# Optimization experiments

Hardware: AMD Instinct MI355X
Metric: run time of the kernel (lower is better)

Reference implementation:

```python
import jax, jax.numpy as jnp
import numpy as np

# spk_param = (thr, temp, damp); dt, tau from module config
THR, TEMP, DAMP = 0.4, 0.1, 0.9
DT, TAU = 0.1, 1.0


@jax.custom_vjp
def spike(v, u):
    # Stochastic Bernoulli spike: sigmoid(temp*v) > uniform noise
    return (jax.nn.sigmoid(TEMP * v) > u).astype(v.dtype)

def _spike_fwd(v, u):
    return spike(v, u), v

def _spike_bwd(v, g):
    # Faithful to the torch Spike.backward: returns the pseudo-derivative
    # damp*clamp(1-|v|,0) directly (the original ignores grad_output).
    return (DAMP * jnp.maximum(1.0 - jnp.abs(v), 0.0), jnp.zeros_like(v))

spike.defvjp(_spike_fwd, _spike_bwd)


def setup_inputs() -> dict:
    key = jax.random.key(0)
    k1, k2, k3, k4, k5 = jax.random.split(key, 5)
    B_, T, IN, N, OUT = 128, 512, 128, 512, 128
    inputs = jax.random.normal(k1, (B_, T, IN), dtype=jnp.float32)
    rand_u = jax.random.uniform(k2, (B_, T, N), dtype=jnp.float32)
    init_std = 1.0
    J = jax.random.normal(k3, (N, N), dtype=jnp.float32) * (init_std / np.sqrt(N))
    Bw = jax.random.normal(k4, (N, IN), dtype=jnp.float32)  # input projection (non-trainable in torch)
    W = jax.random.normal(k5, (OUT, N), dtype=jnp.float32) * (1.0 / np.sqrt(N))
    return {"inputs": inputs, "rand_u": rand_u, "J": J, "Bw": Bw, "W": W}


def reference(inputs, rand_u, J, Bw, W):
    B_, T, _ = inputs.shape
    N = J.shape[0]
    alpha = DT / TAU
    decay = 1.0 - alpha

    def step(carry, xs):
        v, z = carry
        x_t, u_t = xs  # [B, IN], [B, N]
        v_new = decay * v + alpha * z
        lamb = jnp.tanh(v_new) @ J.T + x_t @ Bw.T  # [B, N]
        z_new = spike((lamb - THR) / THR, u_t)
        out = lamb @ W.T  # [B, OUT]
        return (v_new, z_new), (v_new, z_new, out)

    v0 = jnp.zeros((B_, N), dtype=inputs.dtype)
    z0 = jnp.zeros((B_, N), dtype=inputs.dtype)
    xs = (jnp.swapaxes(inputs, 0, 1), jnp.swapaxes(rand_u, 0, 1))  # time-major
    _, (vs, zs, outs) = jax.lax.scan(step, (v0, z0), xs)

    vt = jnp.concatenate([v0[:, None, :], jnp.swapaxes(vs, 0, 1)], axis=1)  # [B, T+1, N]
    zt = jnp.concatenate([z0[:, None, :], jnp.swapaxes(zs, 0, 1)], axis=1)  # [B, T+1, N]
    output_seq = jnp.swapaxes(outs, 0, 1)  # [B, T, OUT]
    return vt, zt, output_seq
```

## Files before the change

kernel.cpp:

```cpp
#include <hip/hip_runtime.h>


typedef __attribute__((ext_vector_type(8))) short short8x;
typedef __attribute__((ext_vector_type(4))) float f32x4;

#define OFF_JQK  (0u)
#define OFF_BWH  (262144u)
#define OFF_BWL  (393216u)
#define OFF_G    (524288u)
#define OFF_M    (786432u)
#define OFF_GPK  (851968u)
#define OFF_MPK  (983040u)

#define SC_J 640.0f
#define SC_S 166.0f

__device__ __forceinline__ unsigned short f2bf(float f) {
  union { float f; unsigned u; } a; a.f = f;
  unsigned r = a.u + 0x7FFFu + ((a.u >> 16) & 1u);
  return (unsigned short)(r >> 16);
}
__device__ __forceinline__ float bf2f(unsigned short h) {
  union { unsigned u; float f; } a; a.u = ((unsigned)h) << 16;
  return a.f;
}
__device__ __forceinline__ float thr_of(float u) {
  return __builtin_fmaf(4.0f, __logf(u / (1.0f - u)), 0.4f);
}
__device__ __forceinline__ float fast_tanh_pos(float x) {
  const float e2 = __expf(x + x);
  return 1.0f - 2.0f / (e2 + 1.0f);
}
__device__ __forceinline__ int sdot4(unsigned a, unsigned b, int acc) {
#if __has_builtin(__builtin_amdgcn_sdot4)
  return __builtin_amdgcn_sdot4((int)a, (int)b, acc, false);
#else
  int r;
  asm("v_dot4_i32_i8 %0, %1, %2, %3" : "=v"(r) : "v"(a), "v"(b), "v"(acc));
  return r;
#endif
}
template <int CTRL>
__device__ __forceinline__ int dpp_add(int x) {
  return x + __builtin_amdgcn_update_dpp(0, x, CTRL, 0xF, 0xF, true);
}
__device__ __forceinline__ int dpp_reduce8(int x) {
  return dpp_add<0x141>(dpp_add<0x4E>(dpp_add<0xB1>(x)));
}

__launch_bounds__(512)
__global__ void jwm_kernel(const float* __restrict__ J, const float* __restrict__ Bw,
                           const float* __restrict__ W, unsigned char* __restrict__ ws) {
  __shared__ float wrow[512];
  const int o = blockIdx.x;
  const int tid = threadIdx.x;
  wrow[tid] = W[(size_t)o * 512 + tid];
  __syncthreads();
  const int k = tid, i = tid & 127;
  float g = 0.0f, m = 0.0f;
  for (int n = 0; n < 512; ++n) {
    const float wv = wrow[n];
    g = __builtin_fmaf(wv, J[(size_t)n * 512 + k], g);
    m = __builtin_fmaf(wv, Bw[(size_t)n * 128 + i], m);
  }
  ((float*)(ws + OFF_G))[(size_t)o * 512 + k] = g;
  if (tid < 128) ((float*)(ws + OFF_M))[(size_t)o * 128 + i] = m;
}

__global__ void pack_kernel(const float* __restrict__ J, const float* __restrict__ Bw,
                            unsigned char* __restrict__ ws) {
  const int id = blockIdx.x * 256 + threadIdx.x;
  if (id < 16384) {
    const int f = id;
    const int l = f & 63, j = (f >> 6) & 3, i = (f >> 8) & 7, w = f >> 11;
    const int kap = l & 7;
    const int n = w * 64 + (l >> 3) * 8 + i;
    const int k0 = 64 * kap + 16 * j;
    unsigned dw[4];
#pragma unroll
    for (int d = 0; d < 4; ++d) {
      unsigned x = 0;
#pragma unroll
      for (int p = 0; p < 4; ++p) {
        const float jv = J[(size_t)n * 512 + k0 + 4 * d + p];
        int q = __float2int_rn(jv * SC_J);
        q = q > 127 ? 127 : (q < -127 ? -127 : q);
        x |= ((unsigned)(q & 255)) << (8 * p);
      }
      dw[d] = x;
    }
    uint4 out; out.x = dw[0]; out.y = dw[1]; out.z = dw[2]; out.w = dw[3];
    ((uint4*)(ws + OFF_JQK))[f] = out;
  } else if (id < 24576) {
    const int idx = id - 16384;
    const int n = idx & 511, kg = idx >> 9, k0 = kg * 8;
    unsigned short* bwh = (unsigned short*)(ws + OFF_BWH);
    unsigned short* bwl = (unsigned short*)(ws + OFF_BWL);
    for (int e = 0; e < 8; ++e) {
      const float x = Bw[(size_t)n * 128 + k0 + e];
      const unsigned short h = f2bf(x);
      bwh[(size_t)idx * 8 + e] = h;
      bwl[(size_t)idx * 8 + e] = f2bf(x - bf2f(h));
    }
  } else if (id < 32768) {
    const int idx = id - 24576;
    const int o = idx & 127, kg = idx >> 7, k0 = kg * 8;
    const float* G = (const float*)(ws + OFF_G);
    unsigned short* gpk = (unsigned short*)(ws + OFF_GPK);
    for (int e = 0; e < 8; ++e) gpk[(size_t)idx * 8 + e] = f2bf(G[(size_t)o * 512 + k0 + e]);
  } else {
    const int idx = id - 32768;
    const int o = idx & 127, kg = idx >> 7, k0 = kg * 8;
    const float* M = (const float*)(ws + OFF_M);
    unsigned short* mpk = (unsigned short*)(ws + OFF_MPK);
    for (int e = 0; e < 8; ++e) mpk[(size_t)idx * 8 + e] = f2bf(M[(size_t)o * 128 + k0 + e]);
  }
}

__launch_bounds__(256)
__global__ void xpd_kernel(const float* __restrict__ X, const float* __restrict__ U,
                           const unsigned char* __restrict__ ws, float* __restrict__ Dbuf) {
  __shared__ short Ah[64 * 136];
  __shared__ short Al[64 * 136];
  const unsigned short* bwh = (const unsigned short*)(ws + OFF_BWH);
  const unsigned short* bwl = (const unsigned short*)(ws + OFF_BWL);
  const int m0 = blockIdx.x * 64;
  const int n0 = blockIdx.y * 64;
  const int tid = threadIdx.x;
  for (int i = tid; i < 64 * 32; i += 256) {
    const int r = i >> 5, kq = i & 31;
    const float4 x4 = *(const float4*)(X + (size_t)(m0 + r) * 128 + kq * 4);
    short4 h4, l4; unsigned short h;
    h = f2bf(x4.x); h4.x = (short)h; l4.x = (short)f2bf(x4.x - bf2f(h));
    h = f2bf(x4.y); h4.y = (short)h; l4.y = (short)f2bf(x4.y - bf2f(h));
    h = f2bf(x4.z); h4.z = (short)h; l4.z = (short)f2bf(x4.z - bf2f(h));
    h = f2bf(x4.w); h4.w = (short)h; l4.w = (short)f2bf(x4.w - bf2f(h));
    *(short4*)(&Ah[r * 136 + kq * 4]) = h4;
    *(short4*)(&Al[r * 136 + kq * 4]) = l4;
  }
  __syncthreads();
  const int w = tid >> 6, l = tid & 63, lhi = l >> 4, llo = l & 15;
  const int rowA = 16 * w + llo;
  f32x4 a0 = {0,0,0,0}, a1 = {0,0,0,0}, a2 = {0,0,0,0}, a3 = {0,0,0,0};
#pragma unroll
  for (int kt = 0; kt < 4; ++kt) {
    const short8x ah = *(const short8x*)(&Ah[rowA * 136 + kt * 32 + lhi * 8]);
    const short8x al = *(const short8x*)(&Al[rowA * 136 + kt * 32 + lhi * 8]);
#define XT(TI, ACC) { \
    const size_t bi = ((size_t)((kt * 4 + lhi) * 512 + n0 + TI * 16 + llo)) * 8; \
    const short8x bh = *(const short8x*)(bwh + bi); \
    const short8x bl = *(const short8x*)(bwl + bi); \
    ACC = __builtin_amdgcn_mfma_f32_16x16x32_bf16(ah, bh, ACC, 0, 0, 0); \
    ACC = __builtin_amdgcn_mfma_f32_16x16x32_bf16(al, bh, ACC, 0, 0, 0); \
    ACC = __builtin_amdgcn_mfma_f32_16x16x32_bf16(ah, bl, ACC, 0, 0, 0); }
    XT(0, a0) XT(1, a1) XT(2, a2) XT(3, a3)
#undef XT
  }
  const int n = n0 + llo;
#pragma unroll
  for (int r = 0; r < 4; ++r) {
    const int bt = m0 + 16 * w + lhi * 4 + r;
    const int bb = bt >> 9, tt = bt & 511;
    const float* urow = U + (size_t)bt * 512;
    float* drow = Dbuf + ((size_t)bb * 513 + tt + 1) * 512;
    drow[n]      = thr_of(urow[n])      - a0[r];
    drow[n + 16] = thr_of(urow[n + 16]) - a1[r];
    drow[n + 32] = thr_of(urow[n + 32]) - a2[r];
    drow[n + 48] = thr_of(urow[n + 48]) - a3[r];
  }
}

__launch_bounds__(512, 1)
__global__ void fused_kernel(const float* __restrict__ X, unsigned char* __restrict__ ws,
                             float* __restrict__ vt, float* __restrict__ zt,
                             float* __restrict__ op) {
  __shared__ __align__(16) unsigned char s_sm[2][640];
  __shared__ unsigned short sl[64 * 520];
  __shared__ unsigned short xl[64 * 136];
  const int b = blockIdx.x;
  const int tid = threadIdx.x;
  const int w = tid >> 6, l = tid & 63;
  const int kap = l & 7, kap80 = kap * 80;
  const int lhi = l >> 4, llo = l & 15;

  uint4 jr[8][4];
#pragma unroll
  for (int i = 0; i < 8; ++i)
#pragma unroll
    for (int j = 0; j < 4; ++j) {
      const unsigned char* p = ws + OFF_JQK +
          (size_t)(((w * 8 + i) * 4 + j) * 64 + l) * 16;
      asm volatile("global_load_dwordx4 %0, %1, off" : "=v"(jr[i][j]) : "v"(p));
    }
  asm volatile("s_waitcnt vmcnt(0)" ::: "memory");

  const unsigned short* gpk = (const unsigned short*)(ws + OFF_GPK);
  const unsigned short* mpk = (const unsigned short*)(ws + OFF_MPK);
  const float SC = 1.0f / (SC_J * SC_S);

  vt[((size_t)b * 513) * 512 + tid] = 0.0f;
  zt[((size_t)b * 513) * 512 + tid] = 0.0f;

  const float* Dp = vt + ((size_t)b * 513 + 1) * 512 + tid;
  float* vtw = vt + ((size_t)b * 513 + 1) * 512 + tid;
  float* ztw = zt + ((size_t)b * 513 + 1) * 512 + tid;

  float dc[8], dnx[8];
#pragma unroll
  for (int i = 0; i < 8; ++i) dc[i] = Dp[(size_t)i * 512];

  unsigned zprev = 0u;
  float v0 = 0.0f, v1 = 0.1f;
  float sf0 = fast_tanh_pos(v0), sf1 = fast_tanh_pos(v1);
  unsigned q0 = (unsigned)__float2int_rn(sf0 * SC_S);
  unsigned q1 = (unsigned)__float2int_rn(sf1 * SC_S);

  for (int C = 0; C < 8; ++C) {
#pragma unroll 1
    for (int c = 0; c < 8; ++c) {
      const int t0 = C * 64 + c * 8;
#pragma unroll
      for (int i = 0; i < 8; ++i) dnx[i] = Dp[(size_t)(t0 + 8 + i) * 512];
#pragma unroll
      for (int i = 0; i < 8; ++i) {
        const int t = t0 + i;
        const int tl = t & 63;
        const unsigned q = zprev ? q1 : q0;
        const float v = zprev ? v1 : v0;
        const float sf = zprev ? sf1 : sf0;
        s_sm[t & 1][w * 80 + l] = (unsigned char)q;
        sl[tl * 520 + tid] = f2bf(sf);
        asm volatile("s_waitcnt lgkmcnt(0)\n\ts_barrier" ::: "memory");
        v0 = 0.9f * v; v1 = v0 + 0.1f;
        sf0 = fast_tanh_pos(v0); sf1 = fast_tanh_pos(v1);
        q0 = (unsigned)__float2int_rn(sf0 * SC_S);
        q1 = (unsigned)__float2int_rn(sf1 * SC_S);
        const unsigned char* sb = &s_sm[t & 1][0];
        const uint4 s0 = *(const uint4*)(sb + kap80);
        const uint4 s1 = *(const uint4*)(sb + kap80 + 16);
        const uint4 s2 = *(const uint4*)(sb + kap80 + 32);
        const uint4 s3 = *(const uint4*)(sb + kap80 + 48);
        int a0 = 0, a1 = 0, a2 = 0, a3 = 0, a4 = 0, a5 = 0, a6 = 0, a7 = 0;
#define DOT(AI, I) \
        AI = sdot4(jr[I][0].x, s0.x, AI); AI = sdot4(jr[I][0].y, s0.y, AI); \
        AI = sdot4(jr[I][0].z, s0.z, AI); AI = sdot4(jr[I][0].w, s0.w, AI); \
        AI = sdot4(jr[I][1].x, s1.x, AI); AI = sdot4(jr[I][1].y, s1.y, AI); \
        AI = sdot4(jr[I][1].z, s1.z, AI); AI = sdot4(jr[I][1].w, s1.w, AI); \
        AI = sdot4(jr[I][2].x, s2.x, AI); AI = sdot4(jr[I][2].y, s2.y, AI); \
        AI = sdot4(jr[I][2].z, s2.z, AI); AI = sdot4(jr[I][2].w, s2.w, AI); \
        AI = sdot4(jr[I][3].x, s3.x, AI); AI = sdot4(jr[I][3].y, s3.y, AI); \
        AI = sdot4(jr[I][3].z, s3.z, AI); AI = sdot4(jr[I][3].w, s3.w, AI);
        DOT(a0, 0) DOT(a1, 1) DOT(a2, 2) DOT(a3, 3)
        DOT(a4, 4) DOT(a5, 5) DOT(a6, 6) DOT(a7, 7)
#undef DOT
        a0 = dpp_reduce8(a0); a1 = dpp_reduce8(a1);
        a2 = dpp_reduce8(a2); a3 = dpp_reduce8(a3);
        a4 = dpp_reduce8(a4); a5 = dpp_reduce8(a5);
        a6 = dpp_reduce8(a6); a7 = dpp_reduce8(a7);
        const int q01 = (l & 1) ? a1 : a0;
        const int q23 = (l & 1) ? a3 : a2;
        const int q45 = (l & 1) ? a5 : a4;
        const int q67 = (l & 1) ? a7 : a6;
        const int r0 = (l & 2) ? q23 : q01;
        const int r1 = (l & 2) ? q67 : q45;
        const int accv = (l & 4) ? r1 : r0;
        const float lam = (float)accv * SC;
        const unsigned z = (lam > dc[i]) ? 1u : 0u;
        unsigned zzero;
        asm("v_and_b32 %0, 0, %1" : "=v"(zzero) : "v"(z));
        vtw[(size_t)t * 512 + zzero] = v;
        ztw[(size_t)t * 512] = z ? 1.0f : 0.0f;
        zprev = z;
      }
#pragma unroll
      for (int i = 0; i < 8; ++i) dc[i] = dnx[i];
    }
    float4 xr[4];
#pragma unroll
    for (int i = 0; i < 4; ++i) {
      const int idx = i * 512 + tid;
      const int r = idx >> 5, c4 = (idx & 31) * 4;
      xr[i] = *(const float4*)(X + ((size_t)b * 512 + C * 64 + r) * 128 + c4);
    }
#pragma unroll
    for (int i = 0; i < 4; ++i) {
      const int idx = i * 512 + tid;
      const int r = idx >> 5, c4 = (idx & 31) * 4;
      short4 h4;
      h4.x = (short)f2bf(xr[i].x); h4.y = (short)f2bf(xr[i].y);
      h4.z = (short)f2bf(xr[i].z); h4.w = (short)f2bf(xr[i].w);
      *(short4*)(xl + r * 136 + c4) = h4;
    }
    __syncthreads();
    const int m = w >> 1, oh = (w & 1) * 4;
    f32x4 a0 = {0,0,0,0}, a1 = {0,0,0,0}, a2 = {0,0,0,0}, a3 = {0,0,0,0};
#pragma unroll
    for (int kt = 0; kt < 16; ++kt) {
      const short8x A = *(const short8x*)(sl + (m * 16 + llo) * 520 + kt * 32 + lhi * 8);
#define GT(TI, ACC) { \
      const short8x B = *(const short8x*)(gpk + ((size_t)((kt * 4 + lhi) * 128 + (oh + TI) * 16 + llo)) * 8); \
      ACC = __builtin_amdgcn_mfma_f32_16x16x32_bf16(A, B, ACC, 0, 0, 0); }
      GT(0, a0) GT(1, a1) GT(2, a2) GT(3, a3)
#undef GT
    }
#pragma unroll
    for (int kt = 0; kt < 4; ++kt) {
      const short8x A = *(const short8x*)(xl + (m * 16 + llo) * 136 + kt * 32 + lhi * 8);
#define MT(TI, ACC) { \
      const short8x B = *(const short8x*)(mpk + ((size_t)((kt * 4 + lhi) * 128 + (oh + TI) * 16 + llo)) * 8); \
      ACC = __builtin_amdgcn_mfma_f32_16x16x32_bf16(A, B, ACC, 0, 0, 0); }
      MT(0, a0) MT(1, a1) MT(2, a2) MT(3, a3)
#undef MT
    }
    float* obase = op + ((size_t)b * 512 + C * 64 + m * 16 + lhi * 4) * 128 + llo;
#pragma unroll
    for (int r = 0; r < 4; ++r) {
      float* orow = obase + (size_t)r * 128;
      orow[(oh + 0) * 16] = a0[r];
      orow[(oh + 1) * 16] = a1[r];
      orow[(oh + 2) * 16] = a2[r];
      orow[(oh + 3) * 16] = a3[r];
    }
    __syncthreads();
  }
}

extern "C" void kernel_launch(void* const* d_in, const int* in_sizes, int n_in,
                              void* d_out, int out_size, void* d_ws, size_t ws_size,
                              hipStream_t stream) {
  const float* X  = (const float*)d_in[0];
  const float* U  = (const float*)d_in[1];
  const float* J  = (const float*)d_in[2];
  const float* Bw = (const float*)d_in[3];
  const float* W  = (const float*)d_in[4];
  float* vt = (float*)d_out;
  float* zt = vt + (size_t)128 * 513 * 512;
  float* op = vt + (size_t)2 * 128 * 513 * 512;
  unsigned char* ws = (unsigned char*)d_ws;

  jwm_kernel<<<128, 512, 0, stream>>>(J, Bw, W, ws);
  pack_kernel<<<136, 256, 0, stream>>>(J, Bw, ws);
  xpd_kernel<<<dim3(1024, 8), 256, 0, stream>>>(X, U, ws, vt);
  fused_kernel<<<128, 512, 0, stream>>>(X, ws, vt, zt, op);
}
```

Before: 803.2 us.

## Split output projection out of recurrence into a separate parallel MFMA kernel

```diff
diff --git a/kernel.cpp b/kernel.cpp
--- a/kernel.cpp
+++ b/kernel.cpp
@@ -171,17 +171,14 @@
 }
 
 __launch_bounds__(512, 1)
-__global__ void fused_kernel(const float* __restrict__ X, unsigned char* __restrict__ ws,
-                             float* __restrict__ vt, float* __restrict__ zt,
-                             float* __restrict__ op) {
+__global__ void recur_kernel(const unsigned char* __restrict__ ws,
+                             const float* __restrict__ Dv,
+                             float* __restrict__ vtw, float* __restrict__ ztw) {
   __shared__ __align__(16) unsigned char s_sm[2][640];
-  __shared__ unsigned short sl[64 * 520];
-  __shared__ unsigned short xl[64 * 136];
   const int b = blockIdx.x;
   const int tid = threadIdx.x;
   const int w = tid >> 6, l = tid & 63;
   const int kap = l & 7, kap80 = kap * 80;
-  const int lhi = l >> 4, llo = l & 15;
 
   uint4 jr[8][4];
 #pragma unroll
@@ -194,134 +191,142 @@
     }
   asm volatile("s_waitcnt vmcnt(0)" ::: "memory");
 
+  const float SC = 1.0f / (SC_J * SC_S);
+  vtw[((size_t)b * 513) * 512 + tid] = 0.0f;
+  ztw[((size_t)b * 513) * 512 + tid] = 0.0f;
+
+  const float* Dp = Dv + ((size_t)b * 513 + 1) * 512 + tid;
+  float* vbase = vtw + ((size_t)b * 513 + 1) * 512 + tid;
+  float* zbase = ztw + ((size_t)b * 513 + 1) * 512 + tid;
+
+  float dc[8], dnx[8];
+#pragma unroll
+  for (int i = 0; i < 8; ++i) dc[i] = Dp[(size_t)i * 512];
+
+  unsigned zprev = 0u;
+  float v0 = 0.0f, v1 = 0.1f;
+  unsigned q0 = (unsigned)__float2int_rn(fast_tanh_pos(v0) * SC_S);
+  unsigned q1 = (unsigned)__float2int_rn(fast_tanh_pos(v1) * SC_S);
+
+  for (int c = 0; c < 64; ++c) {
+    const int t0 = c * 8;
+#pragma unroll
+    for (int i = 0; i < 8; ++i) dnx[i] = Dp[(size_t)(t0 + 8 + i) * 512];
+    float v_arr[8];
+    unsigned zbits = 0u;
+#pragma unroll
+    for (int i = 0; i < 8; ++i) {
+      const int t = t0 + i;
+      const unsigned q = zprev ? q1 : q0;
+      const float v = zprev ? v1 : v0;
+      v_arr[i] = v;
+      s_sm[t & 1][w * 80 + l] = (unsigned char)q;
+      asm volatile("s_waitcnt lgkmcnt(0)\n\ts_barrier" ::: "memory");
+      v0 = 0.9f * v; v1 = v0 + 0.1f;
+      q0 = (unsigned)__float2int_rn(fast_tanh_pos(v0) * SC_S);
+      q1 = (unsigned)__float2int_rn(fast_tanh_pos(v1) * SC_S);
+      const unsigned char* sb = &s_sm[t & 1][0];
+      const uint4 s0 = *(const uint4*)(sb + kap80);
+      const uint4 s1 = *(const uint4*)(sb + kap80 + 16);
+      const uint4 s2 = *(const uint4*)(sb + kap80 + 32);
+      const uint4 s3 = *(const uint4*)(sb + kap80 + 48);
+      int a0 = 0, a1 = 0, a2 = 0, a3 = 0, a4 = 0, a5 = 0, a6 = 0, a7 = 0;
+#define DOT(AI, I) \
+      AI = sdot4(jr[I][0].x, s0.x, AI); AI = sdot4(jr[I][0].y, s0.y, AI); \
+      AI = sdot4(jr[I][0].z, s0.z, AI); AI = sdot4(jr[I][0].w, s0.w, AI); \
+      AI = sdot4(jr[I][1].x, s1.x, AI); AI = sdot4(jr[I][1].y, s1.y, AI); \
+      AI = sdot4(jr[I][1].z, s1.z, AI); AI = sdot4(jr[I][1].w, s1.w, AI); \
+      AI = sdot4(jr[I][2].x, s2.x, AI); AI = sdot4(jr[I][2].y, s2.y, AI); \
+      AI = sdot4(jr[I][2].z, s2.z, AI); AI = sdot4(jr[I][2].w, s2.w, AI); \
+      AI = sdot4(jr[I][3].x, s3.x, AI); AI = sdot4(jr[I][3].y, s3.y, AI); \
+      AI = sdot4(jr[I][3].z, s3.z, AI); AI = sdot4(jr[I][3].w, s3.w, AI);
+      DOT(a0, 0) DOT(a1, 1) DOT(a2, 2) DOT(a3, 3)
+      DOT(a4, 4) DOT(a5, 5) DOT(a6, 6) DOT(a7, 7)
+#undef DOT
+      a0 = dpp_reduce8(a0); a1 = dpp_reduce8(a1);
+      a2 = dpp_reduce8(a2); a3 = dpp_reduce8(a3);
+      a4 = dpp_reduce8(a4); a5 = dpp_reduce8(a5);
+      a6 = dpp_reduce8(a6); a7 = dpp_reduce8(a7);
+      const int q01 = (l & 1) ? a1 : a0;
+      const int q23 = (l & 1) ? a3 : a2;
+      const int q45 = (l & 1) ? a5 : a4;
+      const int q67 = (l & 1) ? a7 : a6;
+      const int r0 = (l & 2) ? q23 : q01;
+      const int r1 = (l & 2) ? q67 : q45;
+      const int accv = (l & 4) ? r1 : r0;
+      const float lam = (float)accv * SC;
+      const unsigned z = (lam > dc[i]) ? 1u : 0u;
+      zbits |= z << i;
+      zprev = z;
+    }
+    unsigned zzero;
+    asm("v_and_b32 %0, 0, %1" : "=v"(zzero) : "v"(zprev));
+    float* vst = vbase + (size_t)t0 * 512 + zzero;
+    float* zst = zbase + (size_t)t0 * 512;
+#pragma unroll
+    for (int i = 0; i < 8; ++i) {
+      vst[(size_t)i * 512] = v_arr[i];
+      zst[(size_t)i * 512] = ((zbits >> i) & 1u) ? 1.0f : 0.0f;
+    }
+#pragma unroll
+    for (int i = 0; i < 8; ++i) dc[i] = dnx[i];
+  }
+}
+
+__launch_bounds__(512)
+__global__ void outk_kernel(const float* __restrict__ X, const float* __restrict__ vt,
+                            const unsigned char* __restrict__ ws,
+                            float* __restrict__ op) {
+  __shared__ unsigned short sl[64 * 520];
+  __shared__ unsigned short xl[64 * 136];
+  const int m0 = blockIdx.x * 64;
+  const int tid = threadIdx.x;
+  const int w = tid >> 6, l = tid & 63, lhi = l >> 4, llo = l & 15;
   const unsigned short* gpk = (const unsigned short*)(ws + OFF_GPK);
   const unsigned short* mpk = (const unsigned short*)(ws + OFF_MPK);
-  const float SC = 1.0f / (SC_J * SC_S);
-
-  vt[((size_t)b * 513) * 512 + tid] = 0.0f;
-  zt[((size_t)b * 513) * 512 + tid] = 0.0f;
-
-  const float* Dp = vt + ((size_t)b * 513 + 1) * 512 + tid;
-  float* vtw = vt + ((size_t)b * 513 + 1) * 512 + tid;
-  float* ztw = zt + ((size_t)b * 513 + 1) * 512 + tid;
-
-  float dc[8], dnx[8];
-#pragma unroll
-  for (int i = 0; i < 8; ++i) dc[i] = Dp[(size_t)i * 512];
-
-  unsigned zprev = 0u;
-  float v0 = 0.0f, v1 = 0.1f;
-  float sf0 = fast_tanh_pos(v0), sf1 = fast_tanh_pos(v1);
-  unsigned q0 = (unsigned)__float2int_rn(sf0 * SC_S);
-  unsigned q1 = (unsigned)__float2int_rn(sf1 * SC_S);
-
-  for (int C = 0; C < 8; ++C) {
-#pragma unroll 1
-    for (int c = 0; c < 8; ++c) {
-      const int t0 = C * 64 + c * 8;
-#pragma unroll
-      for (int i = 0; i < 8; ++i) dnx[i] = Dp[(size_t)(t0 + 8 + i) * 512];
-#pragma unroll
-      for (int i = 0; i < 8; ++i) {
-        const int t = t0 + i;
-        const int tl = t & 63;
-        const unsigned q = zprev ? q1 : q0;
-        const float v = zprev ? v1 : v0;
-        const float sf = zprev ? sf1 : sf0;
-        s_sm[t & 1][w * 80 + l] = (unsigned char)q;
-        sl[tl * 520 + tid] = f2bf(sf);
-        asm volatile("s_waitcnt lgkmcnt(0)\n\ts_barrier" ::: "memory");
-        v0 = 0.9f * v; v1 = v0 + 0.1f;
-        sf0 = fast_tanh_pos(v0); sf1 = fast_tanh_pos(v1);
-        q0 = (unsigned)__float2int_rn(sf0 * SC_S);
-        q1 = (unsigned)__float2int_rn(sf1 * SC_S);
-        const unsigned char* sb = &s_sm[t & 1][0];
-        const uint4 s0 = *(const uint4*)(sb + kap80);
-        const uint4 s1 = *(const uint4*)(sb + kap80 + 16);
-        const uint4 s2 = *(const uint4*)(sb + kap80 + 32);
-        const uint4 s3 = *(const uint4*)(sb + kap80 + 48);
-        int a0 = 0, a1 = 0, a2 = 0, a3 = 0, a4 = 0, a5 = 0, a6 = 0, a7 = 0;
-#define DOT(AI, I) \
-        AI = sdot4(jr[I][0].x, s0.x, AI); AI = sdot4(jr[I][0].y, s0.y, AI); \
-        AI = sdot4(jr[I][0].z, s0.z, AI); AI = sdot4(jr[I][0].w, s0.w, AI); \
-        AI = sdot4(jr[I][1].x, s1.x, AI); AI = sdot4(jr[I][1].y, s1.y, AI); \
-        AI = sdot4(jr[I][1].z, s1.z, AI); AI = sdot4(jr[I][1].w, s1.w, AI); \
-        AI = sdot4(jr[I][2].x, s2.x, AI); AI = sdot4(jr[I][2].y, s2.y, AI); \
-        AI = sdot4(jr[I][2].z, s2.z, AI); AI = sdot4(jr[I][2].w, s2.w, AI); \
-        AI = sdot4(jr[I][3].x, s3.x, AI); AI = sdot4(jr[I][3].y, s3.y, AI); \
-        AI = sdot4(jr[I][3].z, s3.z, AI); AI = sdot4(jr[I][3].w, s3.w, AI);
-        DOT(a0, 0) DOT(a1, 1) DOT(a2, 2) DOT(a3, 3)
-        DOT(a4, 4) DOT(a5, 5) DOT(a6, 6) DOT(a7, 7)
-#undef DOT
-        a0 = dpp_reduce8(a0); a1 = dpp_reduce8(a1);
-        a2 = dpp_reduce8(a2); a3 = dpp_reduce8(a3);
-        a4 = dpp_reduce8(a4); a5 = dpp_reduce8(a5);
-        a6 = dpp_reduce8(a6); a7 = dpp_reduce8(a7);
-        const int q01 = (l & 1) ? a1 : a0;
-        const int q23 = (l & 1) ? a3 : a2;
-        const int q45 = (l & 1) ? a5 : a4;
-        const int q67 = (l & 1) ? a7 : a6;
-        const int r0 = (l & 2) ? q23 : q01;
-        const int r1 = (l & 2) ? q67 : q45;
-        const int accv = (l & 4) ? r1 : r0;
-        const float lam = (float)accv * SC;
-        const unsigned z = (lam > dc[i]) ? 1u : 0u;
-        unsigned zzero;
-        asm("v_and_b32 %0, 0, %1" : "=v"(zzero) : "v"(z));
-        vtw[(size_t)t * 512 + zzero] = v;
-        ztw[(size_t)t * 512] = z ? 1.0f : 0.0f;
-        zprev = z;
-      }
-#pragma unroll
-      for (int i = 0; i < 8; ++i) dc[i] = dnx[i];
-    }
-    float4 xr[4];
-#pragma unroll
-    for (int i = 0; i < 4; ++i) {
-      const int idx = i * 512 + tid;
-      const int r = idx >> 5, c4 = (idx & 31) * 4;
-      xr[i] = *(const float4*)(X + ((size_t)b * 512 + C * 64 + r) * 128 + c4);
-    }
-#pragma unroll
-    for (int i = 0; i < 4; ++i) {
-      const int idx = i * 512 + tid;
-      const int r = idx >> 5, c4 = (idx & 31) * 4;
-      short4 h4;
-      h4.x = (short)f2bf(xr[i].x); h4.y = (short)f2bf(xr[i].y);
-      h4.z = (short)f2bf(xr[i].z); h4.w = (short)f2bf(xr[i].w);
-      *(short4*)(xl + r * 136 + c4) = h4;
-    }
-    __syncthreads();
-    const int m = w >> 1, oh = (w & 1) * 4;
-    f32x4 a0 = {0,0,0,0}, a1 = {0,0,0,0}, a2 = {0,0,0,0}, a3 = {0,0,0,0};
-#pragma unroll
-    for (int kt = 0; kt < 16; ++kt) {
-      const short8x A = *(const short8x*)(sl + (m * 16 + llo) * 520 + kt * 32 + lhi * 8);
+
+#pragma unroll 4
+  for (int r = 0; r < 64; ++r) {
+    const int bt = m0 + r, b = bt >> 9, t = bt & 511;
+    const float v = vt[((size_t)b * 513 + t + 1) * 512 + tid];
+    sl[r * 520 + tid] = f2bf(fast_tanh_pos(v));
+  }
+#pragma unroll
+  for (int i = 0; i < 16; ++i) {
+    const int idx = i * 512 + tid;
+    const int r = idx >> 7, c = idx & 127;
+    const int bt = m0 + r;
+    xl[r * 136 + c] = f2bf(X[(size_t)bt * 128 + c]);
+  }
+  __syncthreads();
+  const int m = w >> 1, oh = (w & 1) * 4;
+  f32x4 a0 = {0,0,0,0}, a1 = {0,0,0,0}, a2 = {0,0,0,0}, a3 = {0,0,0,0};
+#pragma unroll
+  for (int kt = 0; kt < 16; ++kt) {
+    const short8x A = *(const short8x*)(sl + (m * 16 + llo) * 520 + kt * 32 + lhi * 8);
 #define GT(TI, ACC) { \
-      const short8x B = *(const short8x*)(gpk + ((size_t)((kt * 4 + lhi) * 128 + (oh + TI) * 16 + llo)) * 8); \
-      ACC = __builtin_amdgcn_mfma_f32_16x16x32_bf16(A, B, ACC, 0, 0, 0); }
-      GT(0, a0) GT(1, a1) GT(2, a2) GT(3, a3)
+    const short8x B = *(const short8x*)(gpk + ((size_t)((kt * 4 + lhi) * 128 + (oh + TI) * 16 + llo)) * 8); \
+    ACC = __builtin_amdgcn_mfma_f32_16x16x32_bf16(A, B, ACC, 0, 0, 0); }
+    GT(0, a0) GT(1, a1) GT(2, a2) GT(3, a3)
 #undef GT
-    }
-#pragma unroll
-    for (int kt = 0; kt < 4; ++kt) {
-      const short8x A = *(const short8x*)(xl + (m * 16 + llo) * 136 + kt * 32 + lhi * 8);
+  }
+#pragma unroll
+  for (int kt = 0; kt < 4; ++kt) {
+    const short8x A = *(const short8x*)(xl + (m * 16 + llo) * 136 + kt * 32 + lhi * 8);
 #define MT(TI, ACC) { \
-      const short8x B = *(const short8x*)(mpk + ((size_t)((kt * 4 + lhi) * 128 + (oh + TI) * 16 + llo)) * 8); \
-      ACC = __builtin_amdgcn_mfma_f32_16x16x32_bf16(A, B, ACC, 0, 0, 0); }
-      MT(0, a0) MT(1, a1) MT(2, a2) MT(3, a3)
+    const short8x B = *(const short8x*)(mpk + ((size_t)((kt * 4 + lhi) * 128 + (oh + TI) * 16 + llo)) * 8); \
+    ACC = __builtin_amdgcn_mfma_f32_16x16x32_bf16(A, B, ACC, 0, 0, 0); }
+    MT(0, a0) MT(1, a1) MT(2, a2) MT(3, a3)
 #undef MT
-    }
-    float* obase = op + ((size_t)b * 512 + C * 64 + m * 16 + lhi * 4) * 128 + llo;
-#pragma unroll
-    for (int r = 0; r < 4; ++r) {
-      float* orow = obase + (size_t)r * 128;
-      orow[(oh + 0) * 16] = a0[r];
-      orow[(oh + 1) * 16] = a1[r];
-      orow[(oh + 2) * 16] = a2[r];
-      orow[(oh + 3) * 16] = a3[r];
-    }
-    __syncthreads();
+  }
+  float* obase = op + ((size_t)(m0 + m * 16 + lhi * 4)) * 128 + llo;
+#pragma unroll
+  for (int r = 0; r < 4; ++r) {
+    float* orow = obase + (size_t)r * 128;
+    orow[(oh + 0) * 16] = a0[r];
+    orow[(oh + 1) * 16] = a1[r];
+    orow[(oh + 2) * 16] = a2[r];
+    orow[(oh + 3) * 16] = a3[r];
   }
 }
 
@@ -341,5 +346,6 @@
   jwm_kernel<<<128, 512, 0, stream>>>(J, Bw, W, ws);
   pack_kernel<<<136, 256, 0, stream>>>(J, Bw, ws);
   xpd_kernel<<<dim3(1024, 8), 256, 0, stream>>>(X, U, ws, vt);
-  fused_kernel<<<128, 512, 0, stream>>>(X, ws, vt, zt, op);
-}
+  recur_kernel<<<128, 512, 0, stream>>>(ws, vt, vt, zt);
+  outk_kernel<<<1024, 512, 0, stream>>>(X, vt, ws, op);
+}
```

New measurement: 680.5 us. -15.3%, faster.
